# Kernel tuning notes

Measured on AMD Instinct MI355X. Metric: run time of the kernel, lower is better.

The kernel has to match this reference:

```python
import jax, jax.numpy as jnp
import numpy as np

N_NODES = 50000
N_EDGES = 200000
NODE_F = 64
EDGE_F = 16
HID = 32
LAT = 16


def _glorot(key, shape):
    fan_in, fan_out = shape[0], shape[1]
    lim = np.sqrt(6.0 / (fan_in + fan_out))
    return jax.random.uniform(key, shape, jnp.float32, -lim, lim)


def setup_inputs() -> dict:
    key = jax.random.key(0)
    ks = jax.random.split(key, 24)
    inp = {
        "x": jax.random.normal(ks[0], (N_NODES, NODE_F), jnp.float32),
        "edge_index": jax.random.randint(ks[1], (2, N_EDGES), 0, N_NODES, jnp.int64),
        "edge_attr": jax.random.normal(ks[2], (N_EDGES, EDGE_F), jnp.float32),
        # encoder input projection
        "lin_in_w": _glorot(ks[3], (NODE_F, HID)),
        "lin_in_b": jnp.zeros((HID,), jnp.float32),
        # 3 edge MLPs (stacked over layer axis)
        "edge_w1": jnp.stack([_glorot(ks[4 + i], (EDGE_F, HID)) for i in range(3)]),
        "edge_b1": jnp.zeros((3, HID), jnp.float32),
        "edge_w2": jnp.stack([_glorot(ks[7 + i], (HID, HID * HID)) * 0.1 for i in range(3)]),
        "edge_b2": jnp.zeros((3, HID * HID), jnp.float32),
        # 3 NNConv root weights + biases
        "root_w": jnp.stack([_glorot(ks[10 + i], (HID, HID)) for i in range(3)]),
        "root_b": jnp.zeros((3, HID), jnp.float32),
        # encoder output projection
        "lin_out_w": _glorot(ks[13], (HID, LAT)),
        "lin_out_b": jnp.zeros((LAT,), jnp.float32),
        # node decoder MLP
        "dec_w1": _glorot(ks[14], (LAT, HID)),
        "dec_b1": jnp.zeros((HID,), jnp.float32),
        "dec_w2": _glorot(ks[15], (HID, NODE_F)),
        "dec_b2": jnp.zeros((NODE_F,), jnp.float32),
    }
    return inp


def _nnconv(x, src, dst, edge_attr, w1, b1, w2, b2, root_w, root_b):
    # per-edge weight matrix from edge MLP: [E, H, H]
    h = jax.nn.relu(edge_attr @ w1 + b1)
    w_e = (h @ w2 + b2).reshape(-1, HID, HID)
    # gather source features, per-edge matmul: [E, H]
    msg = jnp.einsum("eh,eho->eo", x[src], w_e)
    # scatter-mean to destinations
    agg = jax.ops.segment_sum(msg, dst, num_segments=N_NODES)
    cnt = jax.ops.segment_sum(jnp.ones((msg.shape[0], 1), x.dtype), dst, num_segments=N_NODES)
    agg = agg / jnp.maximum(cnt, 1.0)
    # root weight + bias
    return agg + x @ root_w + root_b


def reference(x, edge_index, edge_attr, lin_in_w, lin_in_b, edge_w1, edge_b1,
              edge_w2, edge_b2, root_w, root_b, lin_out_w, lin_out_b,
              dec_w1, dec_b1, dec_w2, dec_b2):
    src, dst = edge_index[0], edge_index[1]
    h = jax.nn.relu(x @ lin_in_w + lin_in_b)
    for i in range(3):  # fixed number of conv layers (dropout is identity in eval)
        h = _nnconv(h, src, dst, edge_attr, edge_w1[i], edge_b1[i],
                    edge_w2[i], edge_b2[i], root_w[i], root_b[i])
        h = jax.nn.relu(h)
    z = h @ lin_out_w + lin_out_b
    # node decoder
    d = jax.nn.relu(z @ dec_w1 + dec_b1)
    return d @ dec_w2 + dec_b2
```

## Files before the change

### kernel.cpp

```cpp
#include <hip/hip_runtime.h>
#include <hip/hip_bf16.h>
#include <stdint.h>

#define N_NODES 50000
#define N_EDGES 200000
#define NODE_F 64
#define EDGE_F 16
#define HID 32
#define LAT 16
#define KTOT 1056
#define W2A_L 33792
#define SCAN_BLOCKS 196

typedef __attribute__((ext_vector_type(8))) short short8;
typedef __attribute__((ext_vector_type(4))) float f32x4;
typedef __attribute__((ext_vector_type(2))) float f32x2;

static __device__ __forceinline__ unsigned short bfbits(float f) {
  union { __hip_bfloat16 h; unsigned short s; } c; c.h = __float2bfloat16(f); return c.s;
}
static __device__ __forceinline__ unsigned pkt(f32x2 v) {
  return __builtin_amdgcn_perm(__float_as_uint(v.y), __float_as_uint(v.x), 0x07060302u);
}
union AFrag { short8 v; unsigned u[4]; };

__global__ void k_prep(const float* __restrict__ ew2, const float* __restrict__ eb2,
                       const float* __restrict__ ew1,
                       unsigned short* __restrict__ w2a,
                       unsigned short* __restrict__ w1p,
                       int* __restrict__ deg) {
  int g = blockIdx.x*256 + threadIdx.x;
  int l = g / W2A_L;
  int r = g % W2A_L;
  int k = r >> 10;
  int r2 = r & 1023;
  int mt = r2 >> 9;
  int ln = (r2 >> 3) & 63;
  int j  = r2 & 7;
  int h  = (ln >> 4)*8 + j;
  int m  = mt*16 + (ln & 15);
  float v = (k < 32) ? ew2[(size_t)l*32768 + k*1024 + h*32 + m]
                     : eb2[(size_t)l*1024 + h*32 + m];
  w2a[g] = bfbits(v);
  if (g < N_NODES) deg[g] = 0;
  if (g < 3*2*64*8) {
    int l2 = g >> 10;
    int r3 = g & 1023;
    int nt = r3 >> 9;
    int ln2 = (r3 >> 3) & 63;
    int j2  = r3 & 7;
    int kgr = ln2 >> 4;
    float w = (kgr < 2) ? ew1[(size_t)l2*512 + (kgr*8 + j2)*32 + nt*16 + (ln2 & 15)] : 0.f;
    w1p[g] = bfbits(w);
  }
}

__global__ void k_hist(const int* __restrict__ ei, int* __restrict__ deg) {
  int t = blockIdx.x*256 + threadIdx.x;
  if (t >= N_EDGES) return;
  int d = ei[N_EDGES + t];
  d = min(max(d, 0), N_NODES-1);
  atomicAdd(&deg[d], 1);
}

__global__ __launch_bounds__(256) void k_scan1(const int* __restrict__ deg,
                                               int* __restrict__ off,
                                               int* __restrict__ bsum) {
  __shared__ int s[256];
  const int tid = threadIdx.x;
  const int t = blockIdx.x*256 + tid;
  int d = (t < N_NODES) ? deg[t] : 0;
  s[tid] = d; __syncthreads();
  int v = d;
  #pragma unroll
  for (int ofs = 1; ofs < 256; ofs <<= 1) {
    int w = (tid >= ofs) ? s[tid-ofs] : 0;
    __syncthreads();
    v += w; s[tid] = v;
    __syncthreads();
  }
  if (t < N_NODES) off[t] = v - d;
  if (tid == 255) bsum[blockIdx.x] = v;
}

__global__ __launch_bounds__(256) void k_scan23(int* __restrict__ off,
                                                const int* __restrict__ bsum,
                                                int* __restrict__ cursor) {
  __shared__ int sPref;
  const int tid = threadIdx.x;
  const int b = blockIdx.x;
  if (tid < 64) {
    int acc = 0;
    for (int i = tid; i < b; i += 64) acc += bsum[i];
    #pragma unroll
    for (int o = 32; o; o >>= 1) acc += __shfl_down(acc, o);
    if (tid == 0) sPref = acc;
  }
  __syncthreads();
  int pref = sPref;
  int t = b*256 + tid;
  if (t < N_NODES) {
    off[t] += pref;
    cursor[t] = 0;
  }
  if (t == 0) off[N_NODES] = N_EDGES;
}

__global__ void k_scatter(const int* __restrict__ ei, const int* __restrict__ off,
                          int* __restrict__ cursor, int* __restrict__ csr_pos) {
  int t = blockIdx.x*256 + threadIdx.x;
  if (t >= N_EDGES) return;
  int d = ei[N_EDGES + t];
  d = min(max(d, 0), N_NODES-1);
  int pos = atomicAdd(&cursor[d], 1);
  csr_pos[t] = off[d] + pos;
}

__global__ void k_lin_in(const float* __restrict__ x,
                         const float* __restrict__ W,
                         const float* __restrict__ b,
                         float* __restrict__ h) {
  __shared__ float Ws[NODE_F*HID];
  __shared__ float bs[HID];
  for (int i = threadIdx.x; i < NODE_F*HID; i += 256) Ws[i] = W[i];
  if (threadIdx.x < HID) bs[threadIdx.x] = b[threadIdx.x];
  __syncthreads();
  int t = blockIdx.x*256 + threadIdx.x;
  if (t >= N_NODES*HID) return;
  int n = t >> 5, o = t & 31;
  const float4* xp = (const float4*)(x + (size_t)n*NODE_F);
  float acc = bs[o];
  #pragma unroll
  for (int j = 0; j < NODE_F/4; j++) {
    float4 v = xp[j];
    acc = fmaf(v.x, Ws[(4*j+0)*HID+o], acc);
    acc = fmaf(v.y, Ws[(4*j+1)*HID+o], acc);
    acc = fmaf(v.z, Ws[(4*j+2)*HID+o], acc);
    acc = fmaf(v.w, Ws[(4*j+3)*HID+o], acc);
  }
  h[t] = fmaxf(acc, 0.f);
}

__global__ __launch_bounds__(256) void k_msg(const float* __restrict__ hin,
                                             const float* __restrict__ ea,
                                             const int* __restrict__ ei,
                                             const unsigned short* __restrict__ w1pl,
                                             const float* __restrict__ b1,
                                             const unsigned short* __restrict__ w2al,
                                             const int* __restrict__ csr_pos,
                                             unsigned short* __restrict__ msgB) {
  __shared__ float sHE[256*33];
  __shared__ int   sSRC[256];
  __shared__ int   sPOS[256];
  const int tid = threadIdx.x;
  const int be  = blockIdx.x*256;
  const int wv   = tid >> 6;
  const int lane = tid & 63;
  const int nn   = lane & 15;
  const int quad = lane >> 4;
  const int wbase = wv*64;

  {
    int el = wbase + lane;
    int e = min(be + el, N_EDGES-1);
    sSRC[el] = min(max(ei[e], 0), N_NODES-1);
    sPOS[el] = csr_pos[e];
    sHE[el*33 + 32] = 1.0f;
  }

  {
    short8 wb0 = *(const short8*)(w1pl + lane*8);
    short8 wb1 = *(const short8*)(w1pl + 512 + lane*8);
    f32x4 z = {0.f,0.f,0.f,0.f};
    float bv0 = b1[nn], bv1 = b1[nn + 16];
    #pragma unroll
    for (int t = 0; t < 4; t++) {
      AFrag a;
      if (quad < 2) {
        int e = min(be + wbase + t*16 + nn, N_EDGES-1);
        const float4* p = (const float4*)(ea + (size_t)e*EDGE_F + quad*8);
        float4 u = p[0], v = p[1];
        a.u[0] = pkt(f32x2{u.x,u.y}); a.u[1] = pkt(f32x2{u.z,u.w});
        a.u[2] = pkt(f32x2{v.x,v.y}); a.u[3] = pkt(f32x2{v.z,v.w});
      } else {
        #pragma unroll
        for (int i = 0; i < 4; i++) a.u[i] = 0u;
      }
      f32x4 h0 = __builtin_amdgcn_mfma_f32_16x16x32_bf16(a.v, wb0, z, 0, 0, 0);
      f32x4 h1 = __builtin_amdgcn_mfma_f32_16x16x32_bf16(a.v, wb1, z, 0, 0, 0);
      #pragma unroll
      for (int r = 0; r < 4; r++) {
        int ro = (wbase + t*16 + quad*4 + r)*33;
        sHE[ro + nn]      = fmaxf(h0[r] + bv0, 0.f);
        sHE[ro + 16 + nn] = fmaxf(h1[r] + bv1, 0.f);
      }
    }
  }

  short8 bx[4];
  #pragma unroll
  for (int t = 0; t < 4; t++) {
    int si = sSRC[wbase + t*16 + nn];
    const float4* p = (const float4*)(hin + (size_t)si*HID + quad*8);
    float4 a = p[0], b = p[1];
    AFrag f;
    f.u[0] = pkt(f32x2{a.x,a.y}); f.u[1] = pkt(f32x2{a.z,a.w});
    f.u[2] = pkt(f32x2{b.x,b.y}); f.u[3] = pkt(f32x2{b.z,b.w});
    bx[t] = f.v;
  }

  f32x4 c0[4], c1[4];
  #pragma unroll
  for (int t = 0; t < 4; t++) { c0[t] = f32x4{0.f,0.f,0.f,0.f}; c1[t] = c0[t]; }
  const f32x4 zz = {0.f,0.f,0.f,0.f};

  const unsigned short* ap = w2al + (unsigned)lane*8;
  const float* heR[4];
  #pragma unroll
  for (int t = 0; t < 4; t++) heR[t] = sHE + (wbase + t*16 + nn)*33;

  short8 sa0[3], sa1[3];
  float  sh[3][4];
  #pragma unroll
  for (int j = 0; j < 3; j++) {
    sa0[j] = *(const short8*)(ap + j*1024);
    sa1[j] = *(const short8*)(ap + j*1024 + 512);
    #pragma unroll
    for (int t = 0; t < 4; t++) sh[j][t] = heR[t][j];
  }

  #pragma unroll 1
  for (int base = 0; base < 30; base += 3) {
    #pragma unroll
    for (int j = 0; j < 3; j++) {
      const int kk = base + j;
      short8 a0 = sa0[j], a1 = sa1[j];
      #pragma unroll
      for (int t = 0; t < 4; t++) {
        f32x4 u0 = __builtin_amdgcn_mfma_f32_16x16x32_bf16(a0, bx[t], zz, 0, 0, 0);
        f32x4 u1 = __builtin_amdgcn_mfma_f32_16x16x32_bf16(a1, bx[t], zz, 0, 0, 0);
        float hk = sh[j][t];
        #pragma unroll
        for (int r = 0; r < 4; r++) {
          c0[t][r] = fmaf(hk, u0[r], c0[t][r]);
          c1[t][r] = fmaf(hk, u1[r], c1[t][r]);
        }
      }
      sa0[j] = *(const short8*)(ap + (kk+3)*1024);
      sa1[j] = *(const short8*)(ap + (kk+3)*1024 + 512);
      #pragma unroll
      for (int t = 0; t < 4; t++) sh[j][t] = heR[t][kk+3];
    }
  }
  #pragma unroll
  for (int j = 0; j < 3; j++) {
    short8 a0 = sa0[j], a1 = sa1[j];
    #pragma unroll
    for (int t = 0; t < 4; t++) {
      f32x4 u0 = __builtin_amdgcn_mfma_f32_16x16x32_bf16(a0, bx[t], zz, 0, 0, 0);
      f32x4 u1 = __builtin_amdgcn_mfma_f32_16x16x32_bf16(a1, bx[t], zz, 0, 0, 0);
      float hk = sh[j][t];
      #pragma unroll
      for (int r = 0; r < 4; r++) {
        c0[t][r] = fmaf(hk, u0[r], c0[t][r]);
        c1[t][r] = fmaf(hk, u1[r], c1[t][r]);
      }
    }
  }

  #pragma unroll
  for (int t = 0; t < 4; t++) {
    int el = wbase + t*16 + nn;
    if (be + el < N_EDGES) {
      size_t row = (size_t)sPOS[el]*HID;
      unsigned a0 = bfbits(c0[t][0]) | ((unsigned)bfbits(c0[t][1]) << 16);
      unsigned a1 = bfbits(c0[t][2]) | ((unsigned)bfbits(c0[t][3]) << 16);
      unsigned b0 = bfbits(c1[t][0]) | ((unsigned)bfbits(c1[t][1]) << 16);
      unsigned b1v = bfbits(c1[t][2]) | ((unsigned)bfbits(c1[t][3]) << 16);
      *(uint2*)(msgB + row + quad*4)      = make_uint2(a0, a1);
      *(uint2*)(msgB + row + 16 + quad*4) = make_uint2(b0, b1v);
    }
  }
}

__global__ void k_gather(const unsigned short* __restrict__ msgB,
                         const int* __restrict__ off,
                         const float* __restrict__ hin,
                         const float* __restrict__ rw,
                         const float* __restrict__ rb,
                         float* __restrict__ hout) {
  __shared__ float rws[HID*HID];
  __shared__ float rbs[HID];
  for (int i = threadIdx.x; i < HID*HID; i += 256) rws[i] = rw[i];
  if (threadIdx.x < HID) rbs[threadIdx.x] = rb[threadIdx.x];
  __syncthreads();
  int t = blockIdx.x*256 + threadIdx.x;
  if (t >= N_NODES*8) return;
  int n = t >> 3, oc = t & 7;
  int s0 = off[n], s1 = off[n+1];
  float a0 = 0.f, a1 = 0.f, a2 = 0.f, a3 = 0.f;
  for (int j = s0; j < s1; j++) {
    uint2 u = *(const uint2*)(msgB + (size_t)j*HID + oc*4);
    a0 += __uint_as_float(u.x << 16);
    a1 += __uint_as_float(u.x & 0xffff0000u);
    a2 += __uint_as_float(u.y << 16);
    a3 += __uint_as_float(u.y & 0xffff0000u);
  }
  float inv = 1.f / fmaxf((float)(s1 - s0), 1.f);
  a0 = fmaf(a0, inv, rbs[oc*4+0]);
  a1 = fmaf(a1, inv, rbs[oc*4+1]);
  a2 = fmaf(a2, inv, rbs[oc*4+2]);
  a3 = fmaf(a3, inv, rbs[oc*4+3]);
  const float4* hp = (const float4*)(hin + (size_t)n*HID);
  #pragma unroll
  for (int jq = 0; jq < 8; jq++) {
    float4 hv = hp[jq];
    #pragma unroll
    for (int c = 0; c < 4; c++) {
      int j = jq*4 + c;
      float h = (c==0)?hv.x:(c==1)?hv.y:(c==2)?hv.z:hv.w;
      const float4* rp = (const float4*)(rws + j*HID + oc*4);
      float4 r = rp[0];
      a0 = fmaf(h, r.x, a0);
      a1 = fmaf(h, r.y, a1);
      a2 = fmaf(h, r.z, a2);
      a3 = fmaf(h, r.w, a3);
    }
  }
  float4 res = make_float4(fmaxf(a0,0.f), fmaxf(a1,0.f), fmaxf(a2,0.f), fmaxf(a3,0.f));
  ((float4*)(hout + (size_t)n*HID))[oc] = res;
}

__global__ void k_decoder(const float* __restrict__ h,
                          const float* __restrict__ lo_w, const float* __restrict__ lo_b,
                          const float* __restrict__ d1_w, const float* __restrict__ d1_b,
                          const float* __restrict__ d2_w, const float* __restrict__ d2_b,
                          float* __restrict__ out) {
  __shared__ float lows[HID*LAT], lobs[LAT], d1s[LAT*HID], d1bs[HID], d2s[HID*NODE_F], d2bs[NODE_F];
  for (int i = threadIdx.x; i < HID*LAT; i += 256) lows[i] = lo_w[i];
  for (int i = threadIdx.x; i < LAT; i += 256) lobs[i] = lo_b[i];
  for (int i = threadIdx.x; i < LAT*HID; i += 256) d1s[i] = d1_w[i];
  for (int i = threadIdx.x; i < HID; i += 256) d1bs[i] = d1_b[i];
  for (int i = threadIdx.x; i < HID*NODE_F; i += 256) d2s[i] = d2_w[i];
  for (int i = threadIdx.x; i < NODE_F; i += 256) d2bs[i] = d2_b[i];
  __syncthreads();
  int n = blockIdx.x*256 + threadIdx.x;
  if (n >= N_NODES) return;
  float hr[HID];
  const float4* hp = (const float4*)(h + (size_t)n*HID);
  #pragma unroll
  for (int i = 0; i < HID/4; i++) { float4 v = hp[i]; hr[4*i]=v.x; hr[4*i+1]=v.y; hr[4*i+2]=v.z; hr[4*i+3]=v.w; }
  float z[LAT];
  #pragma unroll
  for (int o = 0; o < LAT; o++) {
    float a = lobs[o];
    #pragma unroll
    for (int j = 0; j < HID; j++) a = fmaf(hr[j], lows[j*LAT+o], a);
    z[o] = a;
  }
  float d[HID];
  #pragma unroll
  for (int o = 0; o < HID; o++) {
    float a = d1bs[o];
    #pragma unroll
    for (int j = 0; j < LAT; j++) a = fmaf(z[j], d1s[j*HID+o], a);
    d[o] = fmaxf(a, 0.f);
  }
  float* op = out + (size_t)n*NODE_F;
  #pragma unroll 8
  for (int o = 0; o < NODE_F; o++) {
    float a = d2bs[o];
    #pragma unroll
    for (int j = 0; j < HID; j++) a = fmaf(d[j], d2s[j*NODE_F+o], a);
    op[o] = a;
  }
}

extern "C" void kernel_launch(void* const* d_in, const int* in_sizes, int n_in,
                              void* d_out, int out_size, void* d_ws, size_t ws_size,
                              hipStream_t stream) {
  const float* x   = (const float*)d_in[0];
  const int*   ei  = (const int*)d_in[1];
  const float* ea  = (const float*)d_in[2];
  const float* liw = (const float*)d_in[3];
  const float* lib = (const float*)d_in[4];
  const float* ew1 = (const float*)d_in[5];
  const float* eb1 = (const float*)d_in[6];
  const float* ew2 = (const float*)d_in[7];
  const float* eb2 = (const float*)d_in[8];
  const float* rw  = (const float*)d_in[9];
  const float* rb  = (const float*)d_in[10];
  const float* low = (const float*)d_in[11];
  const float* lob = (const float*)d_in[12];
  const float* d1w = (const float*)d_in[13];
  const float* d1b = (const float*)d_in[14];
  const float* d2w = (const float*)d_in[15];
  const float* d2b = (const float*)d_in[16];
  float* out = (float*)d_out;

  float* h0   = (float*)d_ws;
  float* h1   = h0  + (size_t)N_NODES*HID;
  unsigned short* msgB = (unsigned short*)(h1 + (size_t)N_NODES*HID);
  int*  deg   = (int*)(msgB + (size_t)N_EDGES*HID);
  int*  off   = deg + N_NODES;
  int*  cursor= off + N_NODES + 16;
  int*  cpos  = cursor + N_NODES;
  int*  bsum  = cpos + N_EDGES;
  unsigned short* w2a = (unsigned short*)(bsum + 256);
  unsigned short* w1p = w2a + 3*W2A_L;

  k_prep<<<(3*W2A_L)/256, 256, 0, stream>>>(ew2, eb2, ew1, w2a, w1p, deg);
  k_hist<<<(N_EDGES + 255)/256, 256, 0, stream>>>(ei, deg);
  k_scan1<<<SCAN_BLOCKS, 256, 0, stream>>>(deg, off, bsum);
  k_scan23<<<SCAN_BLOCKS, 256, 0, stream>>>(off, bsum, cursor);
  k_scatter<<<(N_EDGES + 255)/256, 256, 0, stream>>>(ei, off, cursor, cpos);

  k_lin_in<<<(N_NODES*HID + 255)/256, 256, 0, stream>>>(x, liw, lib, h0);

  float* hin = h0; float* hout = h1;
  for (int i = 0; i < 3; i++) {
    k_msg<<<(N_EDGES + 255)/256, 256, 0, stream>>>(hin, ea, ei,
        w1p + (size_t)i*1024, eb1 + i*HID,
        w2a + (size_t)i*W2A_L, cpos, msgB);
    k_gather<<<(N_NODES*8 + 255)/256, 256, 0, stream>>>(msgB, off, hin,
        rw + i*HID*HID, rb + i*HID, hout);
    float* t = hin; hin = hout; hout = t;
  }

  k_decoder<<<(N_NODES + 255)/256, 256, 0, stream>>>(hin, low, lob, d1w, d1b, d2w, d2b, out);
}
```

Measured before the change: 282.7 us.

## Fuse message computation with in-block segmented aggregation over CSR-sorted edges

Edges are now processed in destination-sorted CSR order, so each message block reduces its messages per destination node in shared memory. It writes fp32 sums directly to an aggregation buffer and uses atomics only for nodes whose edges span block boundaries. This removes the bf16 per-edge message buffer round trip and the separate gather pass. The root-weight step becomes a light kernel that also re-zeroes the buffer, and the last layer's root step is folded into the decoder. In exchange it adds sorted-order gathers of edge attributes and source features, plus atomics at block edges.

```diff
diff --git a/kernel.cpp b/kernel.cpp
--- a/kernel.cpp
+++ b/kernel.cpp
@@ -8,7 +8,6 @@
 #define EDGE_F 16
 #define HID 32
 #define LAT 16
-#define KTOT 1056
 #define W2A_L 33792
 #define SCAN_BLOCKS 196
 
@@ -28,7 +27,8 @@
                        const float* __restrict__ ew1,
                        unsigned short* __restrict__ w2a,
                        unsigned short* __restrict__ w1p,
-                       int* __restrict__ deg) {
+                       int* __restrict__ deg,
+                       float* __restrict__ agg) {
   int g = blockIdx.x*256 + threadIdx.x;
   int l = g / W2A_L;
   int r = g % W2A_L;
@@ -43,6 +43,11 @@
                      : eb2[(size_t)l*1024 + h*32 + m];
   w2a[g] = bfbits(v);
   if (g < N_NODES) deg[g] = 0;
+  {
+    float4 z4 = make_float4(0.f,0.f,0.f,0.f);
+    float4* a4 = (float4*)agg;
+    for (int i = g; i < N_NODES*HID/4; i += 101376) a4[i] = z4;
+  }
   if (g < 3*2*64*8) {
     int l2 = g >> 10;
     int r3 = g & 1023;
@@ -107,13 +112,19 @@
 }
 
 __global__ void k_scatter(const int* __restrict__ ei, const int* __restrict__ off,
-                          int* __restrict__ cursor, int* __restrict__ csr_pos) {
+                          int* __restrict__ cursor,
+                          int* __restrict__ csr_src, int* __restrict__ csr_eid,
+                          int* __restrict__ csr_dst) {
   int t = blockIdx.x*256 + threadIdx.x;
   if (t >= N_EDGES) return;
   int d = ei[N_EDGES + t];
   d = min(max(d, 0), N_NODES-1);
-  int pos = atomicAdd(&cursor[d], 1);
-  csr_pos[t] = off[d] + pos;
+  int s = ei[t];
+  s = min(max(s, 0), N_NODES-1);
+  int pos = off[d] + atomicAdd(&cursor[d], 1);
+  csr_src[pos] = s;
+  csr_eid[pos] = t;
+  csr_dst[pos] = d;
 }
 
 __global__ void k_lin_in(const float* __restrict__ x,
@@ -141,17 +152,19 @@
   h[t] = fmaxf(acc, 0.f);
 }
 
-__global__ __launch_bounds__(256) void k_msg(const float* __restrict__ hin,
-                                             const float* __restrict__ ea,
-                                             const int* __restrict__ ei,
-                                             const unsigned short* __restrict__ w1pl,
-                                             const float* __restrict__ b1,
-                                             const unsigned short* __restrict__ w2al,
-                                             const int* __restrict__ csr_pos,
-                                             unsigned short* __restrict__ msgB) {
+__global__ __launch_bounds__(256) void k_msgagg(const float* __restrict__ hin,
+                                                const float* __restrict__ ea,
+                                                const unsigned short* __restrict__ w1pl,
+                                                const float* __restrict__ b1,
+                                                const unsigned short* __restrict__ w2al,
+                                                const int* __restrict__ csr_src,
+                                                const int* __restrict__ csr_eid,
+                                                const int* __restrict__ csr_dst,
+                                                const int* __restrict__ off,
+                                                float* __restrict__ agg) {
   __shared__ float sHE[256*33];
   __shared__ int   sSRC[256];
-  __shared__ int   sPOS[256];
+  __shared__ int   sEID[256];
   const int tid = threadIdx.x;
   const int be  = blockIdx.x*256;
   const int wv   = tid >> 6;
@@ -162,9 +175,9 @@
 
   {
     int el = wbase + lane;
-    int e = min(be + el, N_EDGES-1);
-    sSRC[el] = min(max(ei[e], 0), N_NODES-1);
-    sPOS[el] = csr_pos[e];
+    int pos = min(be + el, N_EDGES-1);
+    sSRC[el] = csr_src[pos];
+    sEID[el] = csr_eid[pos];
     sHE[el*33 + 32] = 1.0f;
   }
 
@@ -177,7 +190,7 @@
     for (int t = 0; t < 4; t++) {
       AFrag a;
       if (quad < 2) {
-        int e = min(be + wbase + t*16 + nn, N_EDGES-1);
+        int e = sEID[wbase + t*16 + nn];
         const float4* p = (const float4*)(ea + (size_t)e*EDGE_F + quad*8);
         float4 u = p[0], v = p[1];
         a.u[0] = pkt(f32x2{u.x,u.y}); a.u[1] = pkt(f32x2{u.z,u.w});
@@ -270,25 +283,48 @@
 
   #pragma unroll
   for (int t = 0; t < 4; t++) {
-    int el = wbase + t*16 + nn;
-    if (be + el < N_EDGES) {
-      size_t row = (size_t)sPOS[el]*HID;
-      unsigned a0 = bfbits(c0[t][0]) | ((unsigned)bfbits(c0[t][1]) << 16);
-      unsigned a1 = bfbits(c0[t][2]) | ((unsigned)bfbits(c0[t][3]) << 16);
-      unsigned b0 = bfbits(c1[t][0]) | ((unsigned)bfbits(c1[t][1]) << 16);
-      unsigned b1v = bfbits(c1[t][2]) | ((unsigned)bfbits(c1[t][3]) << 16);
-      *(uint2*)(msgB + row + quad*4)      = make_uint2(a0, a1);
-      *(uint2*)(msgB + row + 16 + quad*4) = make_uint2(b0, b1v);
+    int ro = (wbase + t*16 + nn)*33 + quad*4;
+    sHE[ro + 0]  = c0[t][0]; sHE[ro + 1]  = c0[t][1];
+    sHE[ro + 2]  = c0[t][2]; sHE[ro + 3]  = c0[t][3];
+    sHE[ro + 16] = c1[t][0]; sHE[ro + 17] = c1[t][1];
+    sHE[ro + 18] = c1[t][2]; sHE[ro + 19] = c1[t][3];
+  }
+  __syncthreads();
+
+  const int s    = be;
+  const int wend = s + 256;
+  const int nF = csr_dst[min(s,       N_EDGES-1)];
+  const int nL = csr_dst[min(s + 255, N_EDGES-1)];
+  for (int basei = 0; basei <= nL - nF; basei += 32) {
+    int idx = basei + (tid >> 3);
+    int n = nF + idx;
+    if (n <= nL) {
+      int oc = tid & 7;
+      int s0 = off[n], s1 = off[n+1];
+      int lo = max(s0, s) - s;
+      int hi = min(s1, wend) - s;
+      float a0 = 0.f, a1 = 0.f, a2 = 0.f, a3 = 0.f;
+      for (int j = lo; j < hi; j++) {
+        const float* row = sHE + j*33 + oc*4;
+        a0 += row[0]; a1 += row[1]; a2 += row[2]; a3 += row[3];
+      }
+      float* dst = agg + (size_t)n*HID + oc*4;
+      if (s0 >= s && s1 <= wend) {
+        *(float4*)dst = make_float4(a0, a1, a2, a3);
+      } else {
+        atomicAdd(dst + 0, a0); atomicAdd(dst + 1, a1);
+        atomicAdd(dst + 2, a2); atomicAdd(dst + 3, a3);
+      }
     }
   }
 }
 
-__global__ void k_gather(const unsigned short* __restrict__ msgB,
-                         const int* __restrict__ off,
-                         const float* __restrict__ hin,
-                         const float* __restrict__ rw,
-                         const float* __restrict__ rb,
-                         float* __restrict__ hout) {
+__global__ void k_root(float* __restrict__ agg,
+                       const int* __restrict__ off,
+                       const float* __restrict__ hin,
+                       const float* __restrict__ rw,
+                       const float* __restrict__ rb,
+                       float* __restrict__ hout) {
   __shared__ float rws[HID*HID];
   __shared__ float rbs[HID];
   for (int i = threadIdx.x; i < HID*HID; i += 256) rws[i] = rw[i];
@@ -297,20 +333,13 @@
   int t = blockIdx.x*256 + threadIdx.x;
   if (t >= N_NODES*8) return;
   int n = t >> 3, oc = t & 7;
-  int s0 = off[n], s1 = off[n+1];
-  float a0 = 0.f, a1 = 0.f, a2 = 0.f, a3 = 0.f;
-  for (int j = s0; j < s1; j++) {
-    uint2 u = *(const uint2*)(msgB + (size_t)j*HID + oc*4);
-    a0 += __uint_as_float(u.x << 16);
-    a1 += __uint_as_float(u.x & 0xffff0000u);
-    a2 += __uint_as_float(u.y << 16);
-    a3 += __uint_as_float(u.y & 0xffff0000u);
-  }
-  float inv = 1.f / fmaxf((float)(s1 - s0), 1.f);
-  a0 = fmaf(a0, inv, rbs[oc*4+0]);
-  a1 = fmaf(a1, inv, rbs[oc*4+1]);
-  a2 = fmaf(a2, inv, rbs[oc*4+2]);
-  a3 = fmaf(a3, inv, rbs[oc*4+3]);
+  float4* ap = (float4*)(agg + (size_t)n*HID);
+  float4 av = ap[oc];
+  float inv = 1.f / fmaxf((float)(off[n+1] - off[n]), 1.f);
+  float a0 = fmaf(av.x, inv, rbs[oc*4+0]);
+  float a1 = fmaf(av.y, inv, rbs[oc*4+1]);
+  float a2 = fmaf(av.z, inv, rbs[oc*4+2]);
+  float a3 = fmaf(av.w, inv, rbs[oc*4+3]);
   const float4* hp = (const float4*)(hin + (size_t)n*HID);
   #pragma unroll
   for (int jq = 0; jq < 8; jq++) {
@@ -327,16 +356,23 @@
       a3 = fmaf(h, r.w, a3);
     }
   }
-  float4 res = make_float4(fmaxf(a0,0.f), fmaxf(a1,0.f), fmaxf(a2,0.f), fmaxf(a3,0.f));
-  ((float4*)(hout + (size_t)n*HID))[oc] = res;
-}
-
-__global__ void k_decoder(const float* __restrict__ h,
+  ((float4*)(hout + (size_t)n*HID))[oc] =
+      make_float4(fmaxf(a0,0.f), fmaxf(a1,0.f), fmaxf(a2,0.f), fmaxf(a3,0.f));
+  ap[oc] = make_float4(0.f, 0.f, 0.f, 0.f);
+}
+
+__global__ void k_decoder(const float* __restrict__ agg,
+                          const int* __restrict__ off,
+                          const float* __restrict__ h,
+                          const float* __restrict__ rw, const float* __restrict__ rb,
                           const float* __restrict__ lo_w, const float* __restrict__ lo_b,
                           const float* __restrict__ d1_w, const float* __restrict__ d1_b,
                           const float* __restrict__ d2_w, const float* __restrict__ d2_b,
                           float* __restrict__ out) {
+  __shared__ float rws[HID*HID], rbs[HID];
   __shared__ float lows[HID*LAT], lobs[LAT], d1s[LAT*HID], d1bs[HID], d2s[HID*NODE_F], d2bs[NODE_F];
+  for (int i = threadIdx.x; i < HID*HID; i += 256) rws[i] = rw[i];
+  for (int i = threadIdx.x; i < HID; i += 256) rbs[i] = rb[i];
   for (int i = threadIdx.x; i < HID*LAT; i += 256) lows[i] = lo_w[i];
   for (int i = threadIdx.x; i < LAT; i += 256) lobs[i] = lo_b[i];
   for (int i = threadIdx.x; i < LAT*HID; i += 256) d1s[i] = d1_w[i];
@@ -346,10 +382,23 @@
   __syncthreads();
   int n = blockIdx.x*256 + threadIdx.x;
   if (n >= N_NODES) return;
+  float hv[HID], av[HID];
+  const float4* hp = (const float4*)(h + (size_t)n*HID);
+  const float4* ap = (const float4*)(agg + (size_t)n*HID);
+  #pragma unroll
+  for (int i = 0; i < HID/4; i++) {
+    float4 v = hp[i]; hv[4*i]=v.x; hv[4*i+1]=v.y; hv[4*i+2]=v.z; hv[4*i+3]=v.w;
+    float4 a = ap[i]; av[4*i]=a.x; av[4*i+1]=a.y; av[4*i+2]=a.z; av[4*i+3]=a.w;
+  }
+  float inv = 1.f / fmaxf((float)(off[n+1] - off[n]), 1.f);
   float hr[HID];
-  const float4* hp = (const float4*)(h + (size_t)n*HID);
-  #pragma unroll
-  for (int i = 0; i < HID/4; i++) { float4 v = hp[i]; hr[4*i]=v.x; hr[4*i+1]=v.y; hr[4*i+2]=v.z; hr[4*i+3]=v.w; }
+  #pragma unroll 4
+  for (int o = 0; o < HID; o++) {
+    float a = fmaf(av[o], inv, rbs[o]);
+    #pragma unroll
+    for (int j = 0; j < HID; j++) a = fmaf(hv[j], rws[j*HID+o], a);
+    hr[o] = fmaxf(a, 0.f);
+  }
   float z[LAT];
   #pragma unroll
   for (int o = 0; o < LAT; o++) {
@@ -400,32 +449,33 @@
 
   float* h0   = (float*)d_ws;
   float* h1   = h0  + (size_t)N_NODES*HID;
-  unsigned short* msgB = (unsigned short*)(h1 + (size_t)N_NODES*HID);
-  int*  deg   = (int*)(msgB + (size_t)N_EDGES*HID);
+  float* agg  = h1  + (size_t)N_NODES*HID;
+  int*  deg   = (int*)(agg + (size_t)N_NODES*HID);
   int*  off   = deg + N_NODES;
   int*  cursor= off + N_NODES + 16;
-  int*  cpos  = cursor + N_NODES;
-  int*  bsum  = cpos + N_EDGES;
+  int*  csrs  = cursor + N_NODES;
+  int*  csre  = csrs + N_EDGES;
+  int*  csrd  = csre + N_EDGES;
+  int*  bsum  = csrd + N_EDGES;
   unsigned short* w2a = (unsigned short*)(bsum + 256);
   unsigned short* w1p = w2a + 3*W2A_L;
 
-  k_prep<<<(3*W2A_L)/256, 256, 0, stream>>>(ew2, eb2, ew1, w2a, w1p, deg);
+  k_prep<<<(3*W2A_L)/256, 256, 0, stream>>>(ew2, eb2, ew1, w2a, w1p, deg, agg);
   k_hist<<<(N_EDGES + 255)/256, 256, 0, stream>>>(ei, deg);
   k_scan1<<<SCAN_BLOCKS, 256, 0, stream>>>(deg, off, bsum);
   k_scan23<<<SCAN_BLOCKS, 256, 0, stream>>>(off, bsum, cursor);
-  k_scatter<<<(N_EDGES + 255)/256, 256, 0, stream>>>(ei, off, cursor, cpos);
+  k_scatter<<<(N_EDGES + 255)/256, 256, 0, stream>>>(ei, off, cursor, csrs, csre, csrd);
 
   k_lin_in<<<(N_NODES*HID + 255)/256, 256, 0, stream>>>(x, liw, lib, h0);
 
-  float* hin = h0; float* hout = h1;
-  for (int i = 0; i < 3; i++) {
-    k_msg<<<(N_EDGES + 255)/256, 256, 0, stream>>>(hin, ea, ei,
-        w1p + (size_t)i*1024, eb1 + i*HID,
-        w2a + (size_t)i*W2A_L, cpos, msgB);
-    k_gather<<<(N_NODES*8 + 255)/256, 256, 0, stream>>>(msgB, off, hin,
-        rw + i*HID*HID, rb + i*HID, hout);
-    float* t = hin; hin = hout; hout = t;
-  }
-
-  k_decoder<<<(N_NODES + 255)/256, 256, 0, stream>>>(hin, low, lob, d1w, d1b, d2w, d2b, out);
-}
+  k_msgagg<<<(N_EDGES + 255)/256, 256, 0, stream>>>(h0, ea, w1p, eb1,
+      w2a, csrs, csre, csrd, off, agg);
+  k_root<<<(N_NODES*8 + 255)/256, 256, 0, stream>>>(agg, off, h0, rw, rb, h1);
+  k_msgagg<<<(N_EDGES + 255)/256, 256, 0, stream>>>(h1, ea, w1p + 1024, eb1 + HID,
+      w2a + (size_t)W2A_L, csrs, csre, csrd, off, agg);
+  k_root<<<(N_NODES*8 + 255)/256, 256, 0, stream>>>(agg, off, h1, rw + HID*HID, rb + HID, h0);
+  k_msgagg<<<(N_EDGES + 255)/256, 256, 0, stream>>>(h0, ea, w1p + 2048, eb1 + 2*HID,
+      w2a + (size_t)2*W2A_L, csrs, csre, csrd, off, agg);
+  k_decoder<<<(N_NODES + 255)/256, 256, 0, stream>>>(agg, off, h0,
+      rw + 2*HID*HID, rb + 2*HID, low, lob, d1w, d1b, d2w, d2b, out);
+}
```

Result: no change. 284.7 us (+0.7%).
